# Optimization experiments

Measured on AMD Instinct MI355X. Metric: run time of the kernel, lower is better.

## Reference

```python
import jax, jax.numpy as jnp
import numpy as np

Z_DIM = 32
POLY_ORDER = 3
INCLUDE_BIAS = True

# Static index arrays replicating the nested-loop term ordering of the torch code.
_I2, _J2 = np.triu_indices(Z_DIM)  # pairs (i, j) with i <= j, row-major in i -> matches loop order
_TRIPLES = np.array([(i, j, k) for i in range(Z_DIM) for j in range(i, Z_DIM) for k in range(j, Z_DIM)], dtype=np.int32)
_TI, _TJ, _TK = _TRIPLES[:, 0], _TRIPLES[:, 1], _TRIPLES[:, 2]


def build_library(z):
    # z: [B, d] -> Theta: [B, n_terms], same column order as build_library_torch
    B = z.shape[0]
    terms = []
    if INCLUDE_BIAS:
        terms.append(jnp.ones((B, 1), dtype=z.dtype))
    terms.append(z)
    if POLY_ORDER >= 2:
        terms.append(z[:, _I2] * z[:, _J2])  # [B, C(d+1,2)] quadratic terms
    if POLY_ORDER >= 3:
        terms.append(z[:, _TI] * z[:, _TJ] * z[:, _TK])  # [B, C(d+2,3)] cubic terms
    return jnp.concatenate(terms, axis=1)


def setup_inputs() -> dict:
    key = jax.random.key(0)
    k1, k2 = jax.random.split(key)
    B = 65536
    n_terms = 6545  # 1 + 32 + 528 + 5984 for d=32, order=3, bias
    z = jax.random.normal(k1, (B, Z_DIM), dtype=jnp.float32)
    Xi = jax.random.normal(k2, (n_terms, Z_DIM), dtype=jnp.float32)
    Xi_mask = jnp.ones((n_terms, Z_DIM), dtype=jnp.float32)
    z_mean = jnp.zeros((1, Z_DIM), dtype=jnp.float32)
    z_std = jnp.ones((1, Z_DIM), dtype=jnp.float32)
    return {"z": z, "Xi": Xi, "Xi_mask": Xi_mask, "z_mean": z_mean, "z_std": z_std}


def reference(z, Xi, Xi_mask, z_mean, z_std):
    # NOTE: the original module computes z_norm = (z - z_mean) / z_std but
    # never uses it; Theta is built from the raw z. Reproduce exactly.
    Theta = build_library(z)            # [B, n_terms]
    Xi_eff = Xi * Xi_mask               # [n_terms, z_dim]
    dz_dt = Theta @ Xi_eff              # [B, z_dim]
    return dz_dt
```

## Files before the change

### kernel.cpp

```cpp
#include <hip/hip_runtime.h>


#define Z 32
#define ROWS 65536
#define NBLK (ROWS / 64)

#define NCHUNK 552
#define NGRAN (NCHUNK * 2)
#define NGP 1120
#define KSPAN 138

typedef float f32x16 __attribute__((ext_vector_type(16)));
typedef _Float16 h2 __attribute__((ext_vector_type(2)));
typedef _Float16 h8 __attribute__((ext_vector_type(8)));

__device__ __forceinline__ h2 pkrtz(float a, float b) {
    return __builtin_bit_cast(h2, __builtin_amdgcn_cvt_pkrtz(a, b));
}

struct Sched {
    unsigned mg[NGP];
    short rt[NGRAN * 8];
    int nq[4];
};

constexpr Sched make_sched() {
    Sched s{};
    short gi[NGP] = {}, gj[NGP] = {};
    char gt[NGP] = {}, gq[NGP] = {};
    int tidx[32][32] = {}, pidx[32] = {};
    {
        int n = 0;
        for (int a = 0; a < 32; ++a)
            for (int b = a; b < 32; ++b) { tidx[a][b] = n; n += 32 - b; }
        for (int i = 0; i < 32; ++i) pidx[i] = i * 32 - i * (i - 1) / 2;
    }
    int g = 0;
    for (int q = 0; q < 4; ++q) {
        int g0 = g;
        for (int b = 0; b < 32; ++b)
            if ((b >> 3) <= q)
                for (int a = 0; a <= b; ++a) { gi[g]=(short)a; gj[g]=(short)b; gt[g]=0; gq[g]=(char)q; ++g; }
        for (int b = 0; b < 32; ++b)
            if ((b >> 3) >= q) { gi[g]=(short)b; gj[g]=32; gt[g]=1; gq[g]=(char)q; ++g; }
        gi[g]=32; gj[g]=32; gt[g]=2; gq[g]=(char)q; ++g;
        while ((g - g0) & 7) { gi[g]=32; gj[g]=32; gt[g]=3; gq[g]=(char)q; ++g; }
        s.nq[q] = (g - g0) / 2;
    }
    for (int gg = 0; gg < NGRAN; ++gg) {
        s.mg[gg] = ((unsigned)gi[gg] * 256u) | (((unsigned)gj[gg] * 256u) << 16);
        int i = gi[gg], j = gj[gg], ty = gt[gg], q = gq[gg];
        for (int jj = 0; jj < 8; ++jj) {
            int k = 8 * q + jj, row = -1;
            if (ty == 0)      { if (k >= j) row = 561 + tidx[i][j] + (k - j); }
            else if (ty == 1) { if (k <= i) row = 33 + pidx[k] + (i - k); }
            else if (ty == 2) { row = 1 + k; }
            s.rt[gg * 8 + jj] = (short)row;
        }
    }
    return s;
}
constexpr Sched S = make_sched();
static_assert(S.nq[0] == 36 && S.nq[1] == 84 && S.nq[2] == 160 && S.nq[3] == 272, "chunk counts");

__global__ void sindy_prep(const float* __restrict__ Xi,
                           const float* __restrict__ Xi_mask,
                           uint2* __restrict__ Bp2, size_t ws_size) {
    __shared__ unsigned short sh[8][32];
    const int tid = threadIdx.x;
    const int jj = tid >> 5, n = tid & 31;
#pragma unroll
    for (int pass = 0; pass < 4; ++pass) {
        int g = blockIdx.x * 4 + pass;
        int row = S.rt[g * 8 + jj];
        float f = 0.0f;
        if (row >= 0) f = Xi[row * Z + n] * Xi_mask[row * Z + n];
        _Float16 hh = (_Float16)f;
        sh[jj][n] = __builtin_bit_cast(unsigned short, hh);
        __syncthreads();
        if (tid < 64) {
            int n2 = tid & 31, rep = tid >> 5;
            unsigned v0 = sh[4*rep+0][n2], v1 = sh[4*rep+1][n2];
            unsigned v2 = sh[4*rep+2][n2], v3 = sh[4*rep+3][n2];
            int c = g >> 1, h = g & 1;
            size_t idx = ((size_t)c * 64 + h * 32 + n2) * 2 + rep;
            if ((idx + 1) * 8 <= ws_size)
                Bp2[idx] = uint2{v0 | (v1 << 16), v2 | (v3 << 16)};
        }
        __syncthreads();
    }
}

__global__ __launch_bounds__(256, 4) void sindy_mfma(const float* __restrict__ z,
                                                     const float* __restrict__ Xi,
                                                     const float* __restrict__ Xi_mask,
                                                     const uint4* __restrict__ Bp,
                                                     float* __restrict__ out) {
    const int lane = threadIdx.x & 63;
    const int kh = threadIdx.x >> 6;
    const int m = lane & 31;
    const int half = lane >> 5;
    const long R = (long)blockIdx.x * 64;

    __shared__ float zs[33][2][32];
    __shared__ float cs[2][32][32];
    __shared__ unsigned mg_sh[NGP];

    for (int t = threadIdx.x; t < NGP; t += 256) mg_sh[t] = S.mg[t];
    for (int idx = threadIdx.x; idx < 512; idx += 256) {
        int row = idx >> 3, q4 = idx & 7;
        float4 v = ((const float4*)(z + (R + row) * Z))[q4];
        int t = row >> 5, mm = row & 31;
        zs[4*q4+0][t][mm] = v.x; zs[4*q4+1][t][mm] = v.y;
        zs[4*q4+2][t][mm] = v.z; zs[4*q4+3][t][mm] = v.w;
    }
    if (threadIdx.x < 64) zs[32][threadIdx.x >> 5][threadIdx.x & 31] = 1.0f;
    __syncthreads();

    const int c0 = kh * KSPAN;
    const char* zmb = (const char*)&zs[0][0][0] + 4 * m;
    const unsigned* mgh = mg_sh + half;
    const uint4* bpl = Bp + lane;

    uint4 bufA = bpl[(size_t)(c0 + 0) * 64];
    uint4 bufB = bpl[(size_t)(c0 + 1) * 64];

    const uint4* bptr = bpl + (size_t)(c0 + 2) * 64;
    const unsigned* mgp = mgh + 2 * c0 + 8;

    unsigned u0 = mgh[2*c0], u1 = mgh[2*c0+2];
    float pA0, pA1, pB0, pB1;
    {
        float i0 = *(const float*)(zmb + (u0 & 0xFFFFu)), i1 = *(const float*)(zmb + (u0 & 0xFFFFu) + 128);
        float j0 = *(const float*)(zmb + (u0 >> 16)),     j1 = *(const float*)(zmb + (u0 >> 16) + 128);
        pA0 = i0 * j0; pA1 = i1 * j1;
        float e0 = *(const float*)(zmb + (u1 & 0xFFFFu)), e1 = *(const float*)(zmb + (u1 & 0xFFFFu) + 128);
        float f0 = *(const float*)(zmb + (u1 >> 16)),     f1 = *(const float*)(zmb + (u1 >> 16) + 128);
        pB0 = e0 * f0; pB1 = e1 * f1;
    }
    unsigned w0s = mgh[2*c0+4], w1s = mgh[2*c0+6];

    f32x16 acc0 = {}, acc1 = {};

    auto seg = [&](int Q, int cbeg, int cfin, bool tail) {
        const char* zq = zmb + Q * 2048;
        h2 zA0, zA1, zA2, zA3, zB0, zB1, zB2, zB3;
        {
            float a0 = *(const float*)(zq +    0), a1 = *(const float*)(zq +  256);
            float a2 = *(const float*)(zq +  512), a3 = *(const float*)(zq +  768);
            float a4 = *(const float*)(zq + 1024), a5 = *(const float*)(zq + 1280);
            float a6 = *(const float*)(zq + 1536), a7 = *(const float*)(zq + 1792);
            float b0 = *(const float*)(zq +  128), b1 = *(const float*)(zq +  384);
            float b2 = *(const float*)(zq +  640), b3 = *(const float*)(zq +  896);
            float b4 = *(const float*)(zq + 1152), b5 = *(const float*)(zq + 1408);
            float b6 = *(const float*)(zq + 1664), b7 = *(const float*)(zq + 1920);
            zA0 = pkrtz(a0, a1); zA1 = pkrtz(a2, a3);
            zA2 = pkrtz(a4, a5); zA3 = pkrtz(a6, a7);
            zB0 = pkrtz(b0, b1); zB1 = pkrtz(b2, b3);
            zB2 = pkrtz(b4, b5); zB3 = pkrtz(b6, b7);
        }

        auto mfma0 = [&](float pp, const uint4& bv) {
            h2 p2 = pkrtz(pp, pp);
            union { h2 h[4]; h8 v; } a;
            a.h[0] = p2 * zA0; a.h[1] = p2 * zA1;
            a.h[2] = p2 * zA2; a.h[3] = p2 * zA3;
            union { uint4 v; h8 h; } b; b.v = bv;
            acc0 = __builtin_amdgcn_mfma_f32_32x32x16_f16(a.v, b.h, acc0, 0, 0, 0);
        };
        auto mfma1 = [&](float pp, const uint4& bv) {
            h2 p2 = pkrtz(pp, pp);
            union { h2 h[4]; h8 v; } a;
            a.h[0] = p2 * zB0; a.h[1] = p2 * zB1;
            a.h[2] = p2 * zB2; a.h[3] = p2 * zB3;
            union { uint4 v; h8 h; } b; b.v = bv;
            acc1 = __builtin_amdgcn_mfma_f32_32x32x16_f16(a.v, b.h, acc1, 0, 0, 0);
        };

        const int cend = tail ? cfin - 2 : cfin;
#pragma unroll 2
        for (int c = cbeg; c < cend; c += 2) {
            uint4 nA = bptr[0];
            uint4 nB = bptr[64];
            bptr += 128;
            unsigned nw0 = mgp[0], nw1 = mgp[2];
            mgp += 4;
            float a0i = *(const float*)(zmb + (w0s & 0xFFFFu));
            float a1i = *(const float*)(zmb + (w0s & 0xFFFFu) + 128);
            float a0j = *(const float*)(zmb + (w0s >> 16));
            float a1j = *(const float*)(zmb + (w0s >> 16) + 128);
            float b0i = *(const float*)(zmb + (w1s & 0xFFFFu));
            float b1i = *(const float*)(zmb + (w1s & 0xFFFFu) + 128);
            float b0j = *(const float*)(zmb + (w1s >> 16));
            float b1j = *(const float*)(zmb + (w1s >> 16) + 128);
            mfma0(pA0, bufA); mfma1(pA1, bufA);
            mfma0(pB0, bufB); mfma1(pB1, bufB);
            pA0 = a0i * a0j; pA1 = a1i * a1j; pB0 = b0i * b0j; pB1 = b1i * b1j;
            w0s = nw0; w1s = nw1;
            bufA = nA; bufB = nB;
        }
        if (tail) {
            mfma0(pA0, bufA); mfma1(pA1, bufA);
            mfma0(pB0, bufB); mfma1(pB1, bufB);
        }
    };

    if (kh == 0)      { seg(0,   0,  36, false); seg(1,  36, 120, false); seg(2, 120, 138, false); }
    else if (kh == 1) { seg(2, 138, 276, false); }
    else if (kh == 2) { seg(2, 276, 280, false); seg(3, 280, 414, false); }
    else              { seg(3, 414, 552, true); }

    if (kh == 3) {
#pragma unroll
        for (int r = 0; r < 16; ++r) {
            int row = (r & 3) + 8 * (r >> 2) + 4 * half;
            cs[0][row][m] = acc0[r]; cs[1][row][m] = acc1[r];
        }
    }
    __syncthreads();
    if (kh == 2) {
#pragma unroll
        for (int r = 0; r < 16; ++r) {
            int row = (r & 3) + 8 * (r >> 2) + 4 * half;
            cs[0][row][m] += acc0[r]; cs[1][row][m] += acc1[r];
        }
    }
    __syncthreads();
    if (kh == 1) {
#pragma unroll
        for (int r = 0; r < 16; ++r) {
            int row = (r & 3) + 8 * (r >> 2) + 4 * half;
            cs[0][row][m] += acc0[r]; cs[1][row][m] += acc1[r];
        }
    }
    __syncthreads();
    if (kh == 0) {
        const float bias = Xi[m] * Xi_mask[m];
        float* o0 = out + R * Z;
        float* o1 = out + (R + 32) * Z;
#pragma unroll
        for (int r = 0; r < 16; ++r) {
            int row = (r & 3) + 8 * (r >> 2) + 4 * half;
            o0[row * Z + m] = acc0[r] + cs[0][row][m] + bias;
            o1[row * Z + m] = acc1[r] + cs[1][row][m] + bias;
        }
    }
}

extern "C" void kernel_launch(void* const* d_in, const int* in_sizes, int n_in,
                              void* d_out, int out_size, void* d_ws, size_t ws_size,
                              hipStream_t stream) {
    const float* z       = (const float*)d_in[0];
    const float* Xi      = (const float*)d_in[1];
    const float* Xi_mask = (const float*)d_in[2];
    float* out = (float*)d_out;
    uint4* Bp  = (uint4*)d_ws;

    sindy_prep<<<NGRAN / 4, 256, 0, stream>>>(Xi, Xi_mask, (uint2*)d_ws, ws_size);
    sindy_mfma<<<NBLK, 256, 0, stream>>>(z, Xi, Xi_mask, Bp, out);
}
```

Measured before the change: 108.9 us.

## Process 128 rows per block with four accumulators to reuse B fragments

Each block now covers 128 rows (four 32-row M tiles) instead of 64, so every B fragment loaded from global memory feeds four MFMAs instead of two. This halves B-operand global traffic per output row and lets the loads be prefetched two steps ahead. The cost is a larger shared-memory footprint, double the accumulator registers (launch bounds lowered to 2 blocks per CU), half as many blocks, and a longer tail handled separately.

```diff
diff --git a/kernel.cpp b/kernel.cpp
--- a/kernel.cpp
+++ b/kernel.cpp
@@ -3,12 +3,11 @@
 
 #define Z 32
 #define ROWS 65536
-#define NBLK (ROWS / 64)
+#define NBLK (ROWS / 128)
 
 #define NCHUNK 552
 #define NGRAN (NCHUNK * 2)
 #define NGP 1120
-#define KSPAN 138
 
 typedef float f32x16 __attribute__((ext_vector_type(16)));
 typedef _Float16 h2 __attribute__((ext_vector_type(2)));
@@ -48,7 +47,7 @@
         s.nq[q] = (g - g0) / 2;
     }
     for (int gg = 0; gg < NGRAN; ++gg) {
-        s.mg[gg] = ((unsigned)gi[gg] * 256u) | (((unsigned)gj[gg] * 256u) << 16);
+        s.mg[gg] = ((unsigned)gi[gg] * 512u) | (((unsigned)gj[gg] * 512u) << 16);
         int i = gi[gg], j = gj[gg], ty = gt[gg], q = gq[gg];
         for (int jj = 0; jj < 8; ++jj) {
             int k = 8 * q + jj, row = -1;
@@ -91,7 +90,7 @@
     }
 }
 
-__global__ __launch_bounds__(256, 4) void sindy_mfma(const float* __restrict__ z,
+__global__ __launch_bounds__(256, 2) void sindy_mfma(const float* __restrict__ z,
                                                      const float* __restrict__ Xi,
                                                      const float* __restrict__ Xi_mask,
                                                      const uint4* __restrict__ Bp,
@@ -100,108 +99,109 @@
     const int kh = threadIdx.x >> 6;
     const int m = lane & 31;
     const int half = lane >> 5;
-    const long R = (long)blockIdx.x * 64;
-
-    __shared__ float zs[33][2][32];
-    __shared__ float cs[2][32][32];
+    const long R = (long)blockIdx.x * 128;
+
+    __shared__ float zs[33][4][32];
+    __shared__ float cs[4][32][32];
     __shared__ unsigned mg_sh[NGP];
 
     for (int t = threadIdx.x; t < NGP; t += 256) mg_sh[t] = S.mg[t];
-    for (int idx = threadIdx.x; idx < 512; idx += 256) {
+    for (int idx = threadIdx.x; idx < 1024; idx += 256) {
         int row = idx >> 3, q4 = idx & 7;
         float4 v = ((const float4*)(z + (R + row) * Z))[q4];
         int t = row >> 5, mm = row & 31;
         zs[4*q4+0][t][mm] = v.x; zs[4*q4+1][t][mm] = v.y;
         zs[4*q4+2][t][mm] = v.z; zs[4*q4+3][t][mm] = v.w;
     }
-    if (threadIdx.x < 64) zs[32][threadIdx.x >> 5][threadIdx.x & 31] = 1.0f;
-    __syncthreads();
-
-    const int c0 = kh * KSPAN;
+    if (threadIdx.x < 128) zs[32][threadIdx.x >> 5][threadIdx.x & 31] = 1.0f;
+    __syncthreads();
+
+    const int c0 = kh * 138;
     const char* zmb = (const char*)&zs[0][0][0] + 4 * m;
     const unsigned* mgh = mg_sh + half;
     const uint4* bpl = Bp + lane;
 
-    uint4 bufA = bpl[(size_t)(c0 + 0) * 64];
-    uint4 bufB = bpl[(size_t)(c0 + 1) * 64];
-
-    const uint4* bptr = bpl + (size_t)(c0 + 2) * 64;
+    auto zprod4 = [&](unsigned ws, float& t0, float& t1, float& t2, float& t3) {
+        const char* bi = zmb + (ws & 0xFFFFu);
+        const char* bj = zmb + (ws >> 16);
+        t0 = *(const float*)(bi +   0) * *(const float*)(bj +   0);
+        t1 = *(const float*)(bi + 128) * *(const float*)(bj + 128);
+        t2 = *(const float*)(bi + 256) * *(const float*)(bj + 256);
+        t3 = *(const float*)(bi + 384) * *(const float*)(bj + 384);
+    };
+
+    uint4 b00 = bpl[(size_t)(c0 + 0) * 64], b01 = bpl[(size_t)(c0 + 1) * 64];
+    uint4 b10 = bpl[(size_t)(c0 + 2) * 64], b11 = bpl[(size_t)(c0 + 3) * 64];
+
+    const uint4* bptr = bpl + (size_t)(c0 + 4) * 64;
     const unsigned* mgp = mgh + 2 * c0 + 8;
 
-    unsigned u0 = mgh[2*c0], u1 = mgh[2*c0+2];
-    float pA0, pA1, pB0, pB1;
+    float pa0, pa1, pa2, pa3, pb0, pb1, pb2, pb3;
     {
-        float i0 = *(const float*)(zmb + (u0 & 0xFFFFu)), i1 = *(const float*)(zmb + (u0 & 0xFFFFu) + 128);
-        float j0 = *(const float*)(zmb + (u0 >> 16)),     j1 = *(const float*)(zmb + (u0 >> 16) + 128);
-        pA0 = i0 * j0; pA1 = i1 * j1;
-        float e0 = *(const float*)(zmb + (u1 & 0xFFFFu)), e1 = *(const float*)(zmb + (u1 & 0xFFFFu) + 128);
-        float f0 = *(const float*)(zmb + (u1 >> 16)),     f1 = *(const float*)(zmb + (u1 >> 16) + 128);
-        pB0 = e0 * f0; pB1 = e1 * f1;
+        unsigned u0 = mgh[2*c0+0], u1 = mgh[2*c0+2];
+        zprod4(u0, pa0, pa1, pa2, pa3);
+        zprod4(u1, pb0, pb1, pb2, pb3);
     }
     unsigned w0s = mgh[2*c0+4], w1s = mgh[2*c0+6];
 
-    f32x16 acc0 = {}, acc1 = {};
+    f32x16 acc0 = {}, acc1 = {}, acc2 = {}, acc3 = {};
 
     auto seg = [&](int Q, int cbeg, int cfin, bool tail) {
-        const char* zq = zmb + Q * 2048;
-        h2 zA0, zA1, zA2, zA3, zB0, zB1, zB2, zB3;
+        const char* zq = zmb + Q * 4096;
+        h2 zt0_0, zt0_1, zt0_2, zt0_3, zt1_0, zt1_1, zt1_2, zt1_3;
+        h2 zt2_0, zt2_1, zt2_2, zt2_3, zt3_0, zt3_1, zt3_2, zt3_3;
         {
-            float a0 = *(const float*)(zq +    0), a1 = *(const float*)(zq +  256);
-            float a2 = *(const float*)(zq +  512), a3 = *(const float*)(zq +  768);
-            float a4 = *(const float*)(zq + 1024), a5 = *(const float*)(zq + 1280);
-            float a6 = *(const float*)(zq + 1536), a7 = *(const float*)(zq + 1792);
-            float b0 = *(const float*)(zq +  128), b1 = *(const float*)(zq +  384);
-            float b2 = *(const float*)(zq +  640), b3 = *(const float*)(zq +  896);
-            float b4 = *(const float*)(zq + 1152), b5 = *(const float*)(zq + 1408);
-            float b6 = *(const float*)(zq + 1664), b7 = *(const float*)(zq + 1920);
-            zA0 = pkrtz(a0, a1); zA1 = pkrtz(a2, a3);
-            zA2 = pkrtz(a4, a5); zA3 = pkrtz(a6, a7);
-            zB0 = pkrtz(b0, b1); zB1 = pkrtz(b2, b3);
-            zB2 = pkrtz(b4, b5); zB3 = pkrtz(b6, b7);
-        }
-
-        auto mfma0 = [&](float pp, const uint4& bv) {
-            h2 p2 = pkrtz(pp, pp);
-            union { h2 h[4]; h8 v; } a;
-            a.h[0] = p2 * zA0; a.h[1] = p2 * zA1;
-            a.h[2] = p2 * zA2; a.h[3] = p2 * zA3;
-            union { uint4 v; h8 h; } b; b.v = bv;
-            acc0 = __builtin_amdgcn_mfma_f32_32x32x16_f16(a.v, b.h, acc0, 0, 0, 0);
+#define LDZ(t) \
+            { float a0 = *(const float*)(zq + (t)*128 +    0), a1 = *(const float*)(zq + (t)*128 +  512); \
+              float a2 = *(const float*)(zq + (t)*128 + 1024), a3 = *(const float*)(zq + (t)*128 + 1536); \
+              float a4 = *(const float*)(zq + (t)*128 + 2048), a5 = *(const float*)(zq + (t)*128 + 2560); \
+              float a6 = *(const float*)(zq + (t)*128 + 3072), a7 = *(const float*)(zq + (t)*128 + 3584); \
+              zt##t##_0 = pkrtz(a0, a1); zt##t##_1 = pkrtz(a2, a3); \
+              zt##t##_2 = pkrtz(a4, a5); zt##t##_3 = pkrtz(a6, a7); }
+            LDZ(0) LDZ(1) LDZ(2) LDZ(3)
+#undef LDZ
+        }
+
+#define MKMFMA(t, accv) \
+        auto mfma##t = [&](float pp, const uint4& bv) { \
+            h2 p2 = pkrtz(pp, pp); \
+            union { h2 h[4]; h8 v; } a; \
+            a.h[0] = p2 * zt##t##_0; a.h[1] = p2 * zt##t##_1; \
+            a.h[2] = p2 * zt##t##_2; a.h[3] = p2 * zt##t##_3; \
+            union { uint4 v; h8 h; } b; b.v = bv; \
+            accv = __builtin_amdgcn_mfma_f32_32x32x16_f16(a.v, b.h, accv, 0, 0, 0); \
         };
-        auto mfma1 = [&](float pp, const uint4& bv) {
-            h2 p2 = pkrtz(pp, pp);
-            union { h2 h[4]; h8 v; } a;
-            a.h[0] = p2 * zB0; a.h[1] = p2 * zB1;
-            a.h[2] = p2 * zB2; a.h[3] = p2 * zB3;
-            union { uint4 v; h8 h; } b; b.v = bv;
-            acc1 = __builtin_amdgcn_mfma_f32_32x32x16_f16(a.v, b.h, acc1, 0, 0, 0);
-        };
-
-        const int cend = tail ? cfin - 2 : cfin;
+        MKMFMA(0, acc0) MKMFMA(1, acc1) MKMFMA(2, acc2) MKMFMA(3, acc3)
+#undef MKMFMA
+
+        const int cend = tail ? cfin - 4 : cfin;
 #pragma unroll 2
         for (int c = cbeg; c < cend; c += 2) {
-            uint4 nA = bptr[0];
-            uint4 nB = bptr[64];
+            uint4 n0 = bptr[0], n1 = bptr[64];
             bptr += 128;
             unsigned nw0 = mgp[0], nw1 = mgp[2];
             mgp += 4;
-            float a0i = *(const float*)(zmb + (w0s & 0xFFFFu));
-            float a1i = *(const float*)(zmb + (w0s & 0xFFFFu) + 128);
-            float a0j = *(const float*)(zmb + (w0s >> 16));
-            float a1j = *(const float*)(zmb + (w0s >> 16) + 128);
-            float b0i = *(const float*)(zmb + (w1s & 0xFFFFu));
-            float b1i = *(const float*)(zmb + (w1s & 0xFFFFu) + 128);
-            float b0j = *(const float*)(zmb + (w1s >> 16));
-            float b1j = *(const float*)(zmb + (w1s >> 16) + 128);
-            mfma0(pA0, bufA); mfma1(pA1, bufA);
-            mfma0(pB0, bufB); mfma1(pB1, bufB);
-            pA0 = a0i * a0j; pA1 = a1i * a1j; pB0 = b0i * b0j; pB1 = b1i * b1j;
+            float qa0, qa1, qa2, qa3, qb0, qb1, qb2, qb3;
+            zprod4(w0s, qa0, qa1, qa2, qa3);
+            zprod4(w1s, qb0, qb1, qb2, qb3);
+            mfma0(pa0, b00); mfma1(pa1, b00); mfma2(pa2, b00); mfma3(pa3, b00);
+            mfma0(pb0, b01); mfma1(pb1, b01); mfma2(pb2, b01); mfma3(pb3, b01);
+            pa0 = qa0; pa1 = qa1; pa2 = qa2; pa3 = qa3;
+            pb0 = qb0; pb1 = qb1; pb2 = qb2; pb3 = qb3;
             w0s = nw0; w1s = nw1;
-            bufA = nA; bufB = nB;
+            b00 = b10; b01 = b11; b10 = n0; b11 = n1;
         }
         if (tail) {
-            mfma0(pA0, bufA); mfma1(pA1, bufA);
-            mfma0(pB0, bufB); mfma1(pB1, bufB);
+            float qa0, qa1, qa2, qa3, qb0, qb1, qb2, qb3;
+            zprod4(w0s, qa0, qa1, qa2, qa3);
+            zprod4(w1s, qb0, qb1, qb2, qb3);
+            mfma0(pa0, b00); mfma1(pa1, b00); mfma2(pa2, b00); mfma3(pa3, b00);
+            mfma0(pb0, b01); mfma1(pb1, b01); mfma2(pb2, b01); mfma3(pb3, b01);
+            pa0 = qa0; pa1 = qa1; pa2 = qa2; pa3 = qa3;
+            pb0 = qb0; pb1 = qb1; pb2 = qb2; pb3 = qb3;
+            b00 = b10; b01 = b11;
+            mfma0(pa0, b00); mfma1(pa1, b00); mfma2(pa2, b00); mfma3(pa3, b00);
+            mfma0(pb0, b01); mfma1(pb1, b01); mfma2(pb2, b01); mfma3(pb3, b01);
         }
     };
 
@@ -215,6 +215,7 @@
         for (int r = 0; r < 16; ++r) {
             int row = (r & 3) + 8 * (r >> 2) + 4 * half;
             cs[0][row][m] = acc0[r]; cs[1][row][m] = acc1[r];
+            cs[2][row][m] = acc2[r]; cs[3][row][m] = acc3[r];
         }
     }
     __syncthreads();
@@ -223,6 +224,7 @@
         for (int r = 0; r < 16; ++r) {
             int row = (r & 3) + 8 * (r >> 2) + 4 * half;
             cs[0][row][m] += acc0[r]; cs[1][row][m] += acc1[r];
+            cs[2][row][m] += acc2[r]; cs[3][row][m] += acc3[r];
         }
     }
     __syncthreads();
@@ -231,18 +233,19 @@
         for (int r = 0; r < 16; ++r) {
             int row = (r & 3) + 8 * (r >> 2) + 4 * half;
             cs[0][row][m] += acc0[r]; cs[1][row][m] += acc1[r];
+            cs[2][row][m] += acc2[r]; cs[3][row][m] += acc3[r];
         }
     }
     __syncthreads();
     if (kh == 0) {
         const float bias = Xi[m] * Xi_mask[m];
-        float* o0 = out + R * Z;
-        float* o1 = out + (R + 32) * Z;
-#pragma unroll
-        for (int r = 0; r < 16; ++r) {
-            int row = (r & 3) + 8 * (r >> 2) + 4 * half;
-            o0[row * Z + m] = acc0[r] + cs[0][row][m] + bias;
-            o1[row * Z + m] = acc1[r] + cs[1][row][m] + bias;
+#pragma unroll
+        for (int r = 0; r < 16; ++r) {
+            int row = (r & 3) + 8 * (r >> 2) + 4 * half;
+            out[(R +  0 + row) * Z + m] = acc0[r] + cs[0][row][m] + bias;
+            out[(R + 32 + row) * Z + m] = acc1[r] + cs[1][row][m] + bias;
+            out[(R + 64 + row) * Z + m] = acc2[r] + cs[2][row][m] + bias;
+            out[(R + 96 + row) * Z + m] = acc3[r] + cs[3][row][m] + bias;
         }
     }
 }
```

Result: no change. 109.5 us (+0.6%).
